# Kernel tuning notes

Measured on AMD Instinct MI355X. Metric: run time of the kernel, lower is better.

Reference implementation:

```python
import jax, jax.numpy as jnp
import numpy as np

B, L, D = 4, 8192, 512
H, G = 8, 4
DH = D // H      # head channels = 64
GC = D // G      # group channels = 128
KSZ = 5          # kernel = offset_range_factor
PAD = KSZ // 2   # = 2; applied to BOTH offset convs (second conv has k=1, pad=2 -> length L+4)


def conv1d(x, w, b, pad):
    # x: (N, Cin, L), w: (Cout, Cin, K) torch layout
    y = jax.lax.conv_general_dilated(x, w, (1,), [(pad, pad)],
                                     dimension_numbers=('NCH', 'OIH', 'NCH'))
    return y + b[None, :, None]


def setup_inputs() -> dict:
    key = jax.random.key(0)
    ks = jax.random.split(key, 9)
    s = 0.02
    p = lambda k, shape: jax.random.normal(k, shape, jnp.float32) * s
    return {
        'x': jax.random.normal(ks[0], (B, L, D), jnp.float32),
        'Wq': p(ks[1], (D, D)), 'bq': jnp.zeros((D,), jnp.float32),
        'Wk': p(ks[2], (D, D)), 'bk': jnp.zeros((D,), jnp.float32),
        'Wv': p(ks[3], (D, D)), 'bv': jnp.zeros((D,), jnp.float32),
        'Woff1': p(ks[4], (GC, GC, KSZ)), 'boff1': jnp.zeros((GC,), jnp.float32),
        'Woff2': p(ks[5], (1, GC, 1)), 'boff2': jnp.zeros((1,), jnp.float32),
        'rel_bias': p(ks[6], (1, D, L)),
        'Wout': p(ks[7], (D, D)), 'bout': jnp.zeros((D,), jnp.float32),
    }


def reference(x, Wq, bq, Wk, bk, Wv, bv, Woff1, boff1, Woff2, boff2, rel_bias, Wout, bout):
    Bv, Lv, Dv = x.shape
    xc = jnp.transpose(x, (0, 2, 1))                         # (B, D, L)
    # 1x1 convs == pointwise linear over channels
    q = jnp.einsum('od,bdl->bol', Wq, xc) + bq[None, :, None]
    # offset prediction on grouped queries
    gq = q.reshape(Bv * G, GC, Lv)                            # (BG, GC, L)
    o = conv1d(gq, Woff1, boff1, PAD)                         # (BG, GC, L)
    o = conv1d(o, Woff2, boff2, PAD)                          # (BG, 1, L+4) due to k=1,pad=2
    offset = jnp.tanh(o[:, 0, :]) * KSZ                       # (BG, L+4)
    n = offset.shape[-1]
    vgrid = jnp.arange(n, dtype=x.dtype) + offset             # (BG, L+4)
    g = 2.0 * vgrid / (n - 1) - 1.0                           # normalized to [-1, 1] over n
    # torch grid_sample, align_corners=False, padding_mode='zeros', H = L
    pos = ((g + 1.0) * Lv - 1.0) / 2.0
    p0 = jnp.floor(pos)
    w1 = pos - p0                                             # weight for upper neighbor
    p0i = p0.astype(jnp.int32)
    p1i = p0i + 1
    feats = xc.reshape(Bv * G, GC, Lv)

    def gather(idx):
        valid = ((idx >= 0) & (idx < Lv)).astype(x.dtype)      # (BG, n)
        idxc = jnp.clip(idx, 0, Lv - 1)
        vals = jnp.take_along_axis(feats, idxc[:, None, :].astype(jnp.int32).repeat(1, axis=1), axis=2) if False else jnp.take_along_axis(feats, jnp.broadcast_to(idxc[:, None, :], (Bv * G, GC, n)), axis=2)
        return vals * valid[:, None, :]

    samp = gather(p0i) * (1.0 - w1)[:, None, :] + gather(p1i) * w1[:, None, :]
    x_sampled = samp[:, :, :Lv].reshape(Bv, Dv, Lv)           # (B, D, L)
    k = jnp.einsum('od,bdl->bol', Wk, x_sampled) + bk[None, :, None]
    v = jnp.einsum('od,bdl->bol', Wv, x_sampled) + bv[None, :, None] + rel_bias
    qh = q.reshape(Bv * H, DH, Lv)
    kh = k.reshape(Bv * H, DH, Lv)
    vh = v.reshape(Bv * H, DH, Lv)
    # channel-attention: contraction over sequence length L
    scores = jnp.einsum('bil,bjl->bij', qh, kh) * (Dv ** -0.5)  # (B*H, DH, DH)
    attn = jax.nn.softmax(scores, axis=-1)
    out = jnp.einsum('bij,bjl->bil', attn, vh)                # (B*H, DH, L)
    # rearrange '(b g) l c -> b c (g l)' with b=B, g=H, l=DH, c=L -> (B, L, D)
    out = jnp.transpose(out.reshape(Bv, H, DH, Lv), (0, 3, 1, 2)).reshape(Bv, Lv, H * DH)
    return out @ Wout.T + bout
```

## Files before the change

### kernel.cpp

```cpp
#include <hip/hip_runtime.h>
#include <hip/hip_bf16.h>
#include <math.h>

using u16 = unsigned short;
using u32 = unsigned int;

typedef __attribute__((ext_vector_type(8))) short s16x8;
typedef __attribute__((ext_vector_type(4))) float f32x4;

#define B_  4
#define L_  8192
#define D_  512
#define H_  8
#define G_  4

__device__ __forceinline__ float bf2f(u16 u) {
    u32 x = ((u32)u) << 16;
    return __uint_as_float(x);
}
__device__ __forceinline__ u16 f2bf(float f) {
    u32 x = __float_as_uint(f);
    u32 lsb = (x >> 16) & 1u;
    x += 0x7FFFu + lsb;
    return (u16)(x >> 16);
}
__device__ __forceinline__ void async16(const void* g, void* l) {
    __builtin_amdgcn_global_load_lds((const __attribute__((address_space(1))) u32*)g,
                                     (__attribute__((address_space(3))) u32*)l, 16, 0, 0);
}

#define CAST_BLOCKS 16384
#define PACK_BLOCKS 384
__global__ __launch_bounds__(256) void prep_kernel(const float* __restrict__ x,
                                                   u16* __restrict__ x_bf,
                                                   const float* __restrict__ Wq,
                                                   const float* __restrict__ Wk,
                                                   const float* __restrict__ Wv,
                                                   u16* __restrict__ Pq,
                                                   u16* __restrict__ Pk,
                                                   u16* __restrict__ Pv,
                                                   const float* __restrict__ W1,
                                                   const float* __restrict__ b1,
                                                   const float* __restrict__ W2,
                                                   const float* __restrict__ b2,
                                                   float* __restrict__ weff) {
    const int bid = blockIdx.x;
    const int tid = threadIdx.x;
    if (bid < CAST_BLOCKS) {
        const int i = bid * 256 + tid;
        float4 v = ((const float4*)x)[i];
        ushort4 o;
        o.x = f2bf(v.x); o.y = f2bf(v.y); o.z = f2bf(v.z); o.w = f2bf(v.w);
        ((ushort4*)x_bf)[i] = o;
    } else if (bid < CAST_BLOCKS + PACK_BLOCKS) {
        const int pb = bid - CAST_BLOCKS;
        const int wsel = pb >> 7;
        const int xb = pb & 127;
        const int g = xb * 4 + (tid >> 6);
        const int lane = tid & 63;
        const int cb = g >> 4, kc = g & 15;
        const int q = lane >> 4, fm = lane & 15;
        const float* W = (wsel == 0) ? Wq : (wsel == 1) ? Wk : Wv;
        u16* P = (wsel == 0) ? Pq : (wsel == 1) ? Pk : Pv;
        const float* src = W + (size_t)(cb * 16 + fm) * 512 + kc * 32 + q * 8;
        float4 a = *(const float4*)src;
        float4 b = *(const float4*)(src + 4);
        ushort4 o0, o1;
        o0.x = f2bf(a.x); o0.y = f2bf(a.y); o0.z = f2bf(a.z); o0.w = f2bf(a.w);
        o1.x = f2bf(b.x); o1.y = f2bf(b.y); o1.z = f2bf(b.z); o1.w = f2bf(b.w);
        u16* dst = P + (size_t)g * 512 + lane * 8;
        *(ushort4*)dst = o0;
        *(ushort4*)(dst + 4) = o1;
    } else {
        const int idx = (bid - CAST_BLOCKS - PACK_BLOCKS) * 256 + tid;
        if (idx < 640) {
            int cin = idx / 5, dk = idx % 5;
            float acc = 0.f;
            for (int c = 0; c < 128; ++c) acc += W2[c] * W1[(c * 128 + cin) * 5 + dk];
            weff[idx] = acc;
        } else if (idx == 640) {
            float s = b2[0];
            for (int c = 0; c < 128; ++c) s += W2[c] * b1[c];
            weff[640] = s;
        } else if (idx == 641) {
            weff[641] = b2[0];
        }
    }
}

__global__ __launch_bounds__(256) void offsets_kernel(const u16* __restrict__ qT,
                                                      const float* __restrict__ weff,
                                                      int* __restrict__ p0o,
                                                      float* __restrict__ w1o) {
    __shared__ u16 qs[128 * 72];
    __shared__ float wf[642];
    __shared__ float red[4][64];
    const int tid = threadIdx.x;
    const int t0 = blockIdx.x * 64;
    const int bg = blockIdx.y;
    const int b = bg >> 2, g = bg & 3;
    for (int i = tid; i < 642; i += 256) wf[i] = weff[i];
    for (int i = tid; i < 128 * 9; i += 256) {
        const int ch = i / 9, seg = i - ch * 9;
        const int l = t0 - 8 + seg * 8;
        s16x8 val = {0, 0, 0, 0, 0, 0, 0, 0};
        if (l >= 0)
            val = *(const s16x8*)(qT + (size_t)(b * D_ + g * 128 + ch) * L_ + l);
        *(s16x8*)(qs + ch * 72 + seg * 8) = val;
    }
    __syncthreads();
    const int w = tid >> 6, lane = tid & 63;
    float acc = 0.f;
    for (int c = 0; c < 32; ++c) {
        const int ch = w * 32 + c;
        const u16* row = qs + ch * 72 + lane + 4;
        const float* wr = wf + ch * 5;
        #pragma unroll
        for (int dk = 0; dk < 5; ++dk) acc += wr[dk] * bf2f(row[dk]);
    }
    red[w][lane] = acc;
    __syncthreads();
    if (w == 0) {
        const float s = red[0][lane] + red[1][lane] + red[2][lane] + red[3][lane];
        const int t = t0 + lane;
        const float o2 = (t >= 2) ? (s + wf[640]) : wf[641];
        const double offv = tanh((double)o2) * 5.0;
        const double vg  = (double)t + offv;
        const double gg  = 2.0 * vg / 8195.0 - 1.0;
        const double pos = ((gg + 1.0) * 8192.0 - 1.0) * 0.5;
        const double p0d = floor(pos);
        p0o[(size_t)bg * L_ + t] = (int)p0d;
        w1o[(size_t)bg * L_ + t] = (float)(pos - p0d);
    }
}

__global__ __launch_bounds__(256) void sample_bf16(const u16* __restrict__ xb,
                                                   const int* __restrict__ p0i,
                                                   const float* __restrict__ w1f,
                                                   u16* __restrict__ xs) {
    const size_t idx = (size_t)blockIdx.x * 256 + threadIdx.x;
    const int d8 = (int)(idx & 63);
    const int t = (int)((idx >> 6) & 8191);
    const int b = (int)(idx >> 19);
    const int g = d8 >> 4;
    const size_t og = (size_t)(b * 4 + g) * L_ + t;
    const int p0 = p0i[og];
    const float w1 = w1f[og];
    const float w0 = 1.f - w1;
    const int p1 = p0 + 1;
    s16x8 a = {0, 0, 0, 0, 0, 0, 0, 0}, c = {0, 0, 0, 0, 0, 0, 0, 0};
    if (p0 >= 0 && p0 < L_) a = *(const s16x8*)(xb + ((size_t)b * L_ + p0) * D_ + d8 * 8);
    if (p1 >= 0 && p1 < L_) c = *(const s16x8*)(xb + ((size_t)b * L_ + p1) * D_ + d8 * 8);
    u16 o[8];
    #pragma unroll
    for (int j = 0; j < 8; ++j)
        o[j] = f2bf(bf2f(((const u16*)&a)[j]) * w0 + bf2f(((const u16*)&c)[j]) * w1);
    *(s16x8*)(xs + idx * 8) = *(const s16x8*)o;
}

__global__ __launch_bounds__(256) void sample_f32(const float* __restrict__ x,
                                                  const int* __restrict__ p0i,
                                                  const float* __restrict__ w1f,
                                                  u16* __restrict__ xs) {
    const size_t idx4 = (size_t)blockIdx.x * 256 + threadIdx.x;
    const int d4 = (int)(idx4 & 127);
    const int t = (int)((idx4 >> 7) & 8191);
    const int b = (int)(idx4 >> 20);
    const int g = d4 >> 5;
    const size_t og = (size_t)(b * 4 + g) * L_ + t;
    const int p0 = p0i[og];
    const float w1 = w1f[og];
    const float w0 = 1.f - w1;
    const int p1 = p0 + 1;
    float4 v0 = {0.f, 0.f, 0.f, 0.f}, v1 = {0.f, 0.f, 0.f, 0.f};
    if (p0 >= 0 && p0 < L_) v0 = *(const float4*)(x + ((size_t)b * L_ + p0) * D_ + d4 * 4);
    if (p1 >= 0 && p1 < L_) v1 = *(const float4*)(x + ((size_t)b * L_ + p1) * D_ + d4 * 4);
    ushort4 o;
    o.x = f2bf(v0.x * w0 + v1.x * w1);
    o.y = f2bf(v0.y * w0 + v1.y * w1);
    o.z = f2bf(v0.z * w0 + v1.z * w1);
    o.w = f2bf(v0.w * w0 + v1.w * w1);
    ((ushort4*)xs)[idx4] = o;
}

template <int MODE>
__global__ __launch_bounds__(256) void gemm_kernel(const u16* __restrict__ A,
                                                   const u16* __restrict__ P0,
                                                   const u16* __restrict__ P1,
                                                   const float* __restrict__ bias0,
                                                   const float* __restrict__ bias1,
                                                   const float* __restrict__ rel,
                                                   void* __restrict__ out0,
                                                   void* __restrict__ out1) {
    __shared__ __align__(16) short abuf[2][128 * 32];
    const int tid = threadIdx.x;
    const int wave = tid >> 6, lane = tid & 63;
    const int bid = blockIdx.x;
    const int xcd = bid & 7;
    const int kk_ = bid >> 3;
    int r0, c0, sel;
    if (MODE == 1) { r0 = (xcd * 32 + (kk_ >> 3)) * 128; sel = (kk_ >> 2) & 1; c0 = (kk_ & 3) * 128; }
    else           { r0 = (xcd * 32 + (kk_ >> 2)) * 128; sel = 0;              c0 = (kk_ & 3) * 128; }
    const u16* P = (MODE == 1 && sel) ? P1 : P0;
    if (MODE == 2) P += (size_t)(r0 >> 13) * 262144;
    const float* bias = (MODE == 1 && sel) ? bias1 : bias0;
    void* out = (MODE == 1 && sel) ? out1 : out0;

    const int wm = (wave >> 1) * 64, wn = (wave & 1) * 64;
    const int srow = lane >> 2;
    const int scol = ((lane & 3) ^ ((srow >> 1) & 3)) * 8;
    const u16* gA = A + (size_t)(r0 + wave * 32) * D_ + scol;
    const int cbase = (c0 + wn) >> 4;

    f32x4 acc[4][4];
    #pragma unroll
    for (int mi = 0; mi < 4; ++mi)
        #pragma unroll
        for (int ni = 0; ni < 4; ++ni) acc[mi][ni] = (f32x4){0.f, 0.f, 0.f, 0.f};

    const int fm = lane & 15;
    const int sblk = ((lane >> 4) ^ ((fm >> 1) & 3)) * 8;

    s16x8 bfrag[4];

    auto stageA = [&](int bsel, int it) {
        const int k0 = it * 32;
        #pragma unroll
        for (int j = 0; j < 2; ++j)
            async16(gA + (size_t)(j * 16 + srow) * D_ + k0,
                    &abuf[bsel][wave * 1024 + j * 512]);
    };
    auto loadB = [&](int it) {
        #pragma unroll
        for (int ni = 0; ni < 4; ++ni)
            bfrag[ni] = *(const s16x8*)(P + ((size_t)((cbase + ni) * 16 + it) * 64 + lane) * 8);
    };

    stageA(0, 0);
    __syncthreads();

    #pragma unroll
    for (int it = 0; it < 16; ++it) {
        const int cur = it & 1;
        loadB(it);
        if (it < 15) stageA(cur ^ 1, it + 1);
        s16x8 af[4];
        #pragma unroll
        for (int mi = 0; mi < 4; ++mi)
            af[mi] = *(const s16x8*)(&abuf[cur][(wm + mi * 16 + fm) * 32 + sblk]);
        #pragma unroll
        for (int mi = 0; mi < 4; ++mi)
            #pragma unroll
            for (int ni = 0; ni < 4; ++ni)
                acc[mi][ni] = __builtin_amdgcn_mfma_f32_16x16x32_bf16(af[mi], bfrag[ni], acc[mi][ni], 0, 0, 0);
        __syncthreads();
    }

    const int fn = lane & 15;
    const int q4 = (lane >> 4) * 4;
    const bool transposed = (MODE == 0) || (MODE == 1 && sel == 0);
    #pragma unroll
    for (int mi = 0; mi < 4; ++mi) {
        #pragma unroll
        for (int ni = 0; ni < 4; ++ni) {
            const int c = c0 + wn + ni * 16 + fn;
            const float bsum = bias[c];
            if (MODE == 2) {
                #pragma unroll
                for (int rg = 0; rg < 4; ++rg) {
                    const int r = r0 + wm + mi * 16 + q4 + rg;
                    ((float*)out)[(size_t)r * D_ + c] = acc[mi][ni][rg] + bsum;
                }
            } else if (transposed) {
                const int r_ = r0 + wm + mi * 16 + q4;
                const int bb = r_ >> 13;
                const int l  = r_ & (L_ - 1);
                ushort4 o;
                o.x = f2bf(acc[mi][ni][0] + bsum);
                o.y = f2bf(acc[mi][ni][1] + bsum);
                o.z = f2bf(acc[mi][ni][2] + bsum);
                o.w = f2bf(acc[mi][ni][3] + bsum);
                *(ushort4*)((u16*)out + (size_t)(bb * D_ + c) * L_ + l) = o;
            } else {
                const int r_ = r0 + wm + mi * 16 + q4;
                const int l  = r_ & (L_ - 1);
                const float4 rl = *(const float4*)(rel + (size_t)c * L_ + l);
                ((u16*)out)[(size_t)(r_ + 0) * D_ + c] = f2bf(acc[mi][ni][0] + bsum + rl.x);
                ((u16*)out)[(size_t)(r_ + 1) * D_ + c] = f2bf(acc[mi][ni][1] + bsum + rl.y);
                ((u16*)out)[(size_t)(r_ + 2) * D_ + c] = f2bf(acc[mi][ni][2] + bsum + rl.z);
                ((u16*)out)[(size_t)(r_ + 3) * D_ + c] = f2bf(acc[mi][ni][3] + bsum + rl.w);
            }
        }
    }
}

__global__ __launch_bounds__(256) void scores_partial(const u16* __restrict__ qT,
                                                      const u16* __restrict__ kT,
                                                      float* __restrict__ part) {
    __shared__ u16 qs[64 * 136];
    __shared__ u16 ks[64 * 136];
    const int chunk = blockIdx.x;
    const int bh = blockIdx.y;
    const int b = bh >> 3, h = bh & 7;
    const int tid = threadIdx.x;
    const int wave = tid >> 6, lane = tid & 63;
    const int wr = (wave >> 1) * 32;
    const int wc = (wave & 1) * 32;
    f32x4 acc[2][2];
    #pragma unroll
    for (int mi = 0; mi < 2; ++mi)
        #pragma unroll
        for (int ni = 0; ni < 2; ++ni) acc[mi][ni] = (f32x4){0.f, 0.f, 0.f, 0.f};
    const size_t base = (size_t)(b * D_ + h * 64) * L_;
    const int m = lane & 15, q = lane >> 4;
    for (int iter = 0; iter < 4; ++iter) {
        const int l0 = chunk * 512 + iter * 128;
        __syncthreads();
        for (int i = tid; i < 1024; i += 256) {
            const int lb = i & 15, ch = i >> 4;
            const size_t gidx = base + (size_t)ch * L_ + l0 + lb * 8;
            *(s16x8*)(qs + ch * 136 + lb * 8) = *(const s16x8*)(qT + gidx);
            *(s16x8*)(ks + ch * 136 + lb * 8) = *(const s16x8*)(kT + gidx);
        }
        __syncthreads();
        #pragma unroll
        for (int kst = 0; kst < 4; ++kst) {
            const int kk = kst * 32 + q * 8;
            s16x8 af[2], bfr[2];
            af[0]  = *(const s16x8*)(qs + (wr + m) * 136 + kk);
            af[1]  = *(const s16x8*)(qs + (wr + 16 + m) * 136 + kk);
            bfr[0] = *(const s16x8*)(ks + (wc + m) * 136 + kk);
            bfr[1] = *(const s16x8*)(ks + (wc + 16 + m) * 136 + kk);
            #pragma unroll
            for (int mi = 0; mi < 2; ++mi)
                #pragma unroll
                for (int ni = 0; ni < 2; ++ni)
                    acc[mi][ni] = __builtin_amdgcn_mfma_f32_16x16x32_bf16(af[mi], bfr[ni], acc[mi][ni], 0, 0, 0);
        }
    }
    float* dst = part + (size_t)(bh * 16 + chunk) * 4096;
    const int q4 = (lane >> 4) * 4;
    #pragma unroll
    for (int mi = 0; mi < 2; ++mi) {
        #pragma unroll
        for (int ni = 0; ni < 2; ++ni) {
            const int j = wc + ni * 16 + m;
            #pragma unroll
            for (int rg = 0; rg < 4; ++rg) {
                const int i = wr + mi * 16 + q4 + rg;
                dst[i * 64 + j] = acc[mi][ni][rg];
            }
        }
    }
}

__global__ __launch_bounds__(256) void softmax_kernel(const float* __restrict__ part,
                                                      float* __restrict__ attn) {
    const int tid = threadIdx.x;
    const int wave = tid >> 6, lane = tid & 63;
    const int row = blockIdx.x * 4 + wave;
    const int bh = row >> 6, i = row & 63;
    float s = 0.f;
    #pragma unroll
    for (int c = 0; c < 16; ++c) s += part[((size_t)(bh * 16 + c)) * 4096 + i * 64 + lane];
    s *= 0.04419417382415922f;
    float m = s;
    for (int off = 32; off > 0; off >>= 1) m = fmaxf(m, __shfl_xor(m, off));
    float e = expf(s - m);
    float sum = e;
    for (int off = 32; off > 0; off >>= 1) sum += __shfl_xor(sum, off);
    attn[(size_t)bh * 4096 + i * 64 + lane] = e / sum;
}

__global__ __launch_bounds__(256) void build_M(const float* __restrict__ Wout,
                                               const float* __restrict__ attn,
                                               u16* __restrict__ Mpack) {
    const int idx = blockIdx.x * 256 + threadIdx.x;
    const int col = idx & 511;
    const int o = (idx >> 9) & 511;
    const int b = idx >> 18;
    const int h = col >> 6, j0 = col & 63;
    const float* wr = Wout + o * 512 + h * 64;
    const float* ar = attn + (size_t)(b * H_ + h) * 4096 + j0;
    float s = 0.f;
    #pragma unroll 8
    for (int i = 0; i < 64; ++i) s += wr[i] * ar[i * 64];
    const int cb = o >> 4, fm = o & 15;
    const int kc = col >> 5, q = (col >> 3) & 3, j = col & 7;
    Mpack[(size_t)b * 262144 + ((size_t)(cb * 16 + kc) * 64 + q * 16 + fm) * 8 + j] = f2bf(s);
}

extern "C" void kernel_launch(void* const* d_in, const int* in_sizes, int n_in,
                              void* d_out, int out_size, void* d_ws, size_t ws_size,
                              hipStream_t stream) {
    const float* x    = (const float*)d_in[0];
    const float* Wq   = (const float*)d_in[1];
    const float* bq   = (const float*)d_in[2];
    const float* Wk   = (const float*)d_in[3];
    const float* bk   = (const float*)d_in[4];
    const float* Wv   = (const float*)d_in[5];
    const float* bv   = (const float*)d_in[6];
    const float* Wo1  = (const float*)d_in[7];
    const float* bo1  = (const float*)d_in[8];
    const float* Wo2  = (const float*)d_in[9];
    const float* bo2  = (const float*)d_in[10];
    const float* rel  = (const float*)d_in[11];
    const float* Wout = (const float*)d_in[12];
    const float* bout = (const float*)d_in[13];

    char* ws = (char*)d_ws;
    const size_t MB = 1024ull * 1024ull;
    const bool big = ws_size >= 165ull * MB;

    u16* x_bf = (u16*)(ws);
    u16* qT   = (u16*)(ws + 32 * MB);
    u16* kT   = (u16*)(ws + 64 * MB);
    u16* v_bf = (u16*)(ws + 96 * MB);

    u16*   xs;
    u16*   Pq; u16* Pk; u16* Pv;
    float* weff; int* p0i; float* w1f;
    float* part; float* attn; u16* Mpack;

    if (big) {
        xs    = (u16*)(ws + 128 * MB);
        part  = (float*)(ws + 128 * MB);
        attn  = (float*)((char*)part + 8 * MB);
        Mpack = (u16*)((char*)attn + 524288);
        Pq    = (u16*)(ws + 160 * MB);
        Pk    = Pq + 262144;
        Pv    = Pk + 262144;
        weff  = (float*)(ws + 162 * MB);
        p0i   = (int*)(ws + 162 * MB + 65536);
        w1f   = (float*)((char*)p0i + 524288);
    } else {
        xs    = x_bf;
        Pq    = (u16*)(ws + 128 * MB);
        Pk    = Pq + 262144;
        Pv    = Pk + 262144;
        weff  = (float*)(ws + 130 * MB);
        p0i   = (int*)(ws + 130 * MB + 65536);
        w1f   = (float*)((char*)p0i + 524288);
        part  = (float*)((char*)w1f + 524288);
        attn  = (float*)((char*)part + 8 * MB);
        Mpack = (u16*)((char*)attn + 524288);
    }

    prep_kernel<<<CAST_BLOCKS + PACK_BLOCKS + 3, 256, 0, stream>>>(
        x, x_bf, Wq, Wk, Wv, Pq, Pk, Pv, Wo1, bo1, Wo2, bo2, weff);
    gemm_kernel<0><<<1024, 256, 0, stream>>>(x_bf, Pq, nullptr, bq, nullptr, nullptr, (void*)qT, nullptr);
    offsets_kernel<<<dim3(128, 16), 256, 0, stream>>>(qT, weff, p0i, w1f);
    if (big) sample_bf16<<<8192, 256, 0, stream>>>(x_bf, p0i, w1f, xs);
    else     sample_f32<<<16384, 256, 0, stream>>>(x, p0i, w1f, xs);
    gemm_kernel<1><<<2048, 256, 0, stream>>>(xs, Pk, Pv, bk, bv, rel, (void*)kT, (void*)v_bf);
    scores_partial<<<dim3(16, 32), 256, 0, stream>>>(qT, kT, part);
    softmax_kernel<<<512, 256, 0, stream>>>(part, attn);
    build_M<<<4096, 256, 0, stream>>>(Wout, attn, Mpack);
    gemm_kernel<2><<<1024, 256, 0, stream>>>(v_bf, Mpack, nullptr, bout, nullptr, nullptr, d_out, nullptr);
}
```

Measured before the change: 382.1 us.

## Stage B tiles through LDS with a 4-slot async pipeline in projection GEMM

The GEMM kernel now copies the packed weight (B) fragments into LDS with async global-to-LDS loads instead of reading them directly into registers each iteration. It also deepens the A/B staging from double buffering to a 4-slot ring that keeps three stages in flight, using explicit vmcnt waits plus raw barriers in place of __syncthreads. The goal is to hide global load latency and share B fragments across waves. In exchange LDS use roughly quadruples, which may lower occupancy, and the hand-coded waitcnt values must exactly match the number of outstanding loads.

```diff
diff --git a/kernel.cpp b/kernel.cpp
--- a/kernel.cpp
+++ b/kernel.cpp
@@ -28,6 +28,9 @@
     __builtin_amdgcn_global_load_lds((const __attribute__((address_space(1))) u32*)g,
                                      (__attribute__((address_space(3))) u32*)l, 16, 0, 0);
 }
+#define WAIT_VM8   0x0F78
+#define WAIT_VM4   0x0F74
+#define WAIT_VM0   0x0F70
 
 #define CAST_BLOCKS 16384
 #define PACK_BLOCKS 384
@@ -192,7 +195,8 @@
                                                    const float* __restrict__ rel,
                                                    void* __restrict__ out0,
                                                    void* __restrict__ out1) {
-    __shared__ __align__(16) short abuf[2][128 * 32];
+    __shared__ __align__(16) short abuf[4][128 * 32];
+    __shared__ __align__(16) short bbuf[4][128 * 32];
     const int tid = threadIdx.x;
     const int wave = tid >> 6, lane = tid & 63;
     const int bid = blockIdx.x;
@@ -210,7 +214,7 @@
     const int srow = lane >> 2;
     const int scol = ((lane & 3) ^ ((srow >> 1) & 3)) * 8;
     const u16* gA = A + (size_t)(r0 + wave * 32) * D_ + scol;
-    const int cbase = (c0 + wn) >> 4;
+    const int cb0 = c0 >> 4;
 
     f32x4 acc[4][4];
     #pragma unroll
@@ -221,39 +225,44 @@
     const int fm = lane & 15;
     const int sblk = ((lane >> 4) ^ ((fm >> 1) & 3)) * 8;
 
-    s16x8 bfrag[4];
-
-    auto stageA = [&](int bsel, int it) {
+    auto stageAB = [&](int slot, int it) {
         const int k0 = it * 32;
         #pragma unroll
         for (int j = 0; j < 2; ++j)
             async16(gA + (size_t)(j * 16 + srow) * D_ + k0,
-                    &abuf[bsel][wave * 1024 + j * 512]);
+                    &abuf[slot][wave * 1024 + j * 512]);
+        #pragma unroll
+        for (int j = 0; j < 2; ++j)
+            async16(P + ((size_t)((cb0 + wave * 2 + j) * 16 + it) * 64 + lane) * 8,
+                    &bbuf[slot][(wave * 2 + j) * 512]);
     };
-    auto loadB = [&](int it) {
+
+    stageAB(0, 0); stageAB(1, 1); stageAB(2, 2);
+    __builtin_amdgcn_s_waitcnt(WAIT_VM8);
+    __builtin_amdgcn_s_barrier();
+
+    #pragma unroll
+    for (int it = 0; it < 16; ++it) {
+        const int slot = it & 3;
+        s16x8 af[4], bf[4];
+        #pragma unroll
+        for (int mi = 0; mi < 4; ++mi)
+            af[mi] = *(const s16x8*)(&abuf[slot][(wm + mi * 16 + fm) * 32 + sblk]);
         #pragma unroll
         for (int ni = 0; ni < 4; ++ni)
-            bfrag[ni] = *(const s16x8*)(P + ((size_t)((cbase + ni) * 16 + it) * 64 + lane) * 8);
-    };
-
-    stageA(0, 0);
-    __syncthreads();
-
-    #pragma unroll
-    for (int it = 0; it < 16; ++it) {
-        const int cur = it & 1;
-        loadB(it);
-        if (it < 15) stageA(cur ^ 1, it + 1);
-        s16x8 af[4];
-        #pragma unroll
-        for (int mi = 0; mi < 4; ++mi)
-            af[mi] = *(const s16x8*)(&abuf[cur][(wm + mi * 16 + fm) * 32 + sblk]);
+            bf[ni] = *(const s16x8*)(&bbuf[slot][((wave & 1) * 4 + ni) * 512 + lane * 8]);
+        if (it < 13) stageAB((it + 3) & 3, it + 3);
         #pragma unroll
         for (int mi = 0; mi < 4; ++mi)
             #pragma unroll
             for (int ni = 0; ni < 4; ++ni)
-                acc[mi][ni] = __builtin_amdgcn_mfma_f32_16x16x32_bf16(af[mi], bfrag[ni], acc[mi][ni], 0, 0, 0);
-        __syncthreads();
+                acc[mi][ni] = __builtin_amdgcn_mfma_f32_16x16x32_bf16(af[mi], bf[ni], acc[mi][ni], 0, 0, 0);
+        if (it < 15) {
+            if (it <= 12)      __builtin_amdgcn_s_waitcnt(WAIT_VM8);
+            else if (it == 13) __builtin_amdgcn_s_waitcnt(WAIT_VM4);
+            else               __builtin_amdgcn_s_waitcnt(WAIT_VM0);
+            __builtin_amdgcn_s_barrier();
+        }
     }
 
     const int fn = lane & 15;
```

After: 375.9 us. Within noise of the previous version (-1.6%).

## Widen GEMM tiles, fuse K and V outputs per block, double K-step

Applied to the files above, without the earlier changes.

The GEMM kernel now computes K and V projections in the same block from one staged A tile, so the sampled input is read once instead of twice. Modes 0 and 2 use 128x256 tiles with 8 N-fragments per wave, and every mode stages 64 K-columns per iteration in two sub-buffers, which halves the number of barriers. Grids shrink to match. The cost is many more accumulator registers per wave (128 f32x4 lanes' worth), which lowers occupancy and may cause spills. Shared memory per block also doubles.

```diff
diff --git a/kernel.cpp b/kernel.cpp
--- a/kernel.cpp
+++ b/kernel.cpp
@@ -192,86 +192,107 @@
                                                    const float* __restrict__ rel,
                                                    void* __restrict__ out0,
                                                    void* __restrict__ out1) {
-    __shared__ __align__(16) short abuf[2][128 * 32];
+    __shared__ __align__(16) short abuf[2][2][128 * 32];
     const int tid = threadIdx.x;
     const int wave = tid >> 6, lane = tid & 63;
     const int bid = blockIdx.x;
     const int xcd = bid & 7;
     const int kk_ = bid >> 3;
-    int r0, c0, sel;
-    if (MODE == 1) { r0 = (xcd * 32 + (kk_ >> 3)) * 128; sel = (kk_ >> 2) & 1; c0 = (kk_ & 3) * 128; }
-    else           { r0 = (xcd * 32 + (kk_ >> 2)) * 128; sel = 0;              c0 = (kk_ & 3) * 128; }
-    const u16* P = (MODE == 1 && sel) ? P1 : P0;
-    if (MODE == 2) P += (size_t)(r0 >> 13) * 262144;
-    const float* bias = (MODE == 1 && sel) ? bias1 : bias0;
-    void* out = (MODE == 1 && sel) ? out1 : out0;
-
-    const int wm = (wave >> 1) * 64, wn = (wave & 1) * 64;
+    int r0, c0;
+    if (MODE == 1) { r0 = (xcd * 32 + (kk_ >> 2)) * 128; c0 = (kk_ & 3) * 128; }
+    else           { r0 = (xcd * 32 + (kk_ >> 1)) * 128; c0 = (kk_ & 1) * 256; }
+    const u16* Pk = P0;
+    if (MODE == 2) Pk += (size_t)(r0 >> 13) * 262144;
+    const u16* Pv = P1;
+
+    const int wm = (wave >> 1) * 64;
+    const int wn = (MODE == 1) ? (wave & 1) * 64 : (wave & 1) * 128;
+    constexpr int NI = (MODE == 1) ? 4 : 8;
+    const int cbase = (c0 + wn) >> 4;
+
     const int srow = lane >> 2;
     const int scol = ((lane & 3) ^ ((srow >> 1) & 3)) * 8;
     const u16* gA = A + (size_t)(r0 + wave * 32) * D_ + scol;
-    const int cbase = (c0 + wn) >> 4;
-
-    f32x4 acc[4][4];
-    #pragma unroll
-    for (int mi = 0; mi < 4; ++mi)
-        #pragma unroll
-        for (int ni = 0; ni < 4; ++ni) acc[mi][ni] = (f32x4){0.f, 0.f, 0.f, 0.f};
-
     const int fm = lane & 15;
     const int sblk = ((lane >> 4) ^ ((fm >> 1) & 3)) * 8;
 
-    s16x8 bfrag[4];
-
-    auto stageA = [&](int bsel, int it) {
-        const int k0 = it * 32;
-        #pragma unroll
-        for (int j = 0; j < 2; ++j)
-            async16(gA + (size_t)(j * 16 + srow) * D_ + k0,
-                    &abuf[bsel][wave * 1024 + j * 512]);
-    };
-    auto loadB = [&](int it) {
-        #pragma unroll
-        for (int ni = 0; ni < 4; ++ni)
-            bfrag[ni] = *(const s16x8*)(P + ((size_t)((cbase + ni) * 16 + it) * 64 + lane) * 8);
+    f32x4 acc[4][NI];
+    #pragma unroll
+    for (int mi = 0; mi < 4; ++mi)
+        #pragma unroll
+        for (int ni = 0; ni < NI; ++ni) acc[mi][ni] = (f32x4){0.f, 0.f, 0.f, 0.f};
+    f32x4 accv[4][(MODE == 1) ? 4 : 1];
+    if (MODE == 1) {
+        #pragma unroll
+        for (int mi = 0; mi < 4; ++mi)
+            #pragma unroll
+            for (int ni = 0; ni < 4; ++ni) accv[mi][ni] = (f32x4){0.f, 0.f, 0.f, 0.f};
+    }
+
+    auto stageA = [&](int buf, int it) {
+        #pragma unroll
+        for (int sub = 0; sub < 2; ++sub)
+            #pragma unroll
+            for (int j = 0; j < 2; ++j)
+                async16(gA + (size_t)(j * 16 + srow) * D_ + it * 64 + sub * 32,
+                        &abuf[buf][sub][wave * 1024 + j * 512]);
     };
 
     stageA(0, 0);
     __syncthreads();
 
     #pragma unroll
-    for (int it = 0; it < 16; ++it) {
+    for (int it = 0; it < 8; ++it) {
         const int cur = it & 1;
-        loadB(it);
-        if (it < 15) stageA(cur ^ 1, it + 1);
-        s16x8 af[4];
-        #pragma unroll
-        for (int mi = 0; mi < 4; ++mi)
-            af[mi] = *(const s16x8*)(&abuf[cur][(wm + mi * 16 + fm) * 32 + sblk]);
-        #pragma unroll
-        for (int mi = 0; mi < 4; ++mi)
-            #pragma unroll
-            for (int ni = 0; ni < 4; ++ni)
-                acc[mi][ni] = __builtin_amdgcn_mfma_f32_16x16x32_bf16(af[mi], bfrag[ni], acc[mi][ni], 0, 0, 0);
+        if (it < 7) stageA(cur ^ 1, it + 1);
+        #pragma unroll
+        for (int sub = 0; sub < 2; ++sub) {
+            const int kc = it * 2 + sub;
+            s16x8 bk[NI];
+            #pragma unroll
+            for (int ni = 0; ni < NI; ++ni)
+                bk[ni] = *(const s16x8*)(Pk + ((size_t)((cbase + ni) * 16 + kc) * 64 + lane) * 8);
+            s16x8 bv[(MODE == 1) ? 4 : 1];
+            if (MODE == 1) {
+                #pragma unroll
+                for (int ni = 0; ni < 4; ++ni)
+                    bv[ni] = *(const s16x8*)(Pv + ((size_t)((cbase + ni) * 16 + kc) * 64 + lane) * 8);
+            }
+            s16x8 af[4];
+            #pragma unroll
+            for (int mi = 0; mi < 4; ++mi)
+                af[mi] = *(const s16x8*)(&abuf[cur][sub][(wm + mi * 16 + fm) * 32 + sblk]);
+            #pragma unroll
+            for (int mi = 0; mi < 4; ++mi)
+                #pragma unroll
+                for (int ni = 0; ni < NI; ++ni)
+                    acc[mi][ni] = __builtin_amdgcn_mfma_f32_16x16x32_bf16(af[mi], bk[ni], acc[mi][ni], 0, 0, 0);
+            if (MODE == 1) {
+                #pragma unroll
+                for (int mi = 0; mi < 4; ++mi)
+                    #pragma unroll
+                    for (int ni = 0; ni < 4; ++ni)
+                        accv[mi][ni] = __builtin_amdgcn_mfma_f32_16x16x32_bf16(af[mi], bv[ni], accv[mi][ni], 0, 0, 0);
+            }
+        }
         __syncthreads();
     }
 
     const int fn = lane & 15;
     const int q4 = (lane >> 4) * 4;
-    const bool transposed = (MODE == 0) || (MODE == 1 && sel == 0);
     #pragma unroll
     for (int mi = 0; mi < 4; ++mi) {
         #pragma unroll
-        for (int ni = 0; ni < 4; ++ni) {
+        for (int ni = 0; ni < NI; ++ni) {
             const int c = c0 + wn + ni * 16 + fn;
-            const float bsum = bias[c];
+            const float bsum = bias0[c];
             if (MODE == 2) {
                 #pragma unroll
                 for (int rg = 0; rg < 4; ++rg) {
                     const int r = r0 + wm + mi * 16 + q4 + rg;
-                    ((float*)out)[(size_t)r * D_ + c] = acc[mi][ni][rg] + bsum;
+                    ((float*)out0)[(size_t)r * D_ + c] = acc[mi][ni][rg] + bsum;
                 }
-            } else if (transposed) {
+            } else {
                 const int r_ = r0 + wm + mi * 16 + q4;
                 const int bb = r_ >> 13;
                 const int l  = r_ & (L_ - 1);
@@ -280,15 +301,24 @@
                 o.y = f2bf(acc[mi][ni][1] + bsum);
                 o.z = f2bf(acc[mi][ni][2] + bsum);
                 o.w = f2bf(acc[mi][ni][3] + bsum);
-                *(ushort4*)((u16*)out + (size_t)(bb * D_ + c) * L_ + l) = o;
-            } else {
+                *(ushort4*)((u16*)out0 + (size_t)(bb * D_ + c) * L_ + l) = o;
+            }
+        }
+    }
+    if (MODE == 1) {
+        #pragma unroll
+        for (int mi = 0; mi < 4; ++mi) {
+            #pragma unroll
+            for (int ni = 0; ni < 4; ++ni) {
+                const int c = c0 + wn + ni * 16 + fn;
+                const float bsum = bias1[c];
                 const int r_ = r0 + wm + mi * 16 + q4;
                 const int l  = r_ & (L_ - 1);
                 const float4 rl = *(const float4*)(rel + (size_t)c * L_ + l);
-                ((u16*)out)[(size_t)(r_ + 0) * D_ + c] = f2bf(acc[mi][ni][0] + bsum + rl.x);
-                ((u16*)out)[(size_t)(r_ + 1) * D_ + c] = f2bf(acc[mi][ni][1] + bsum + rl.y);
-                ((u16*)out)[(size_t)(r_ + 2) * D_ + c] = f2bf(acc[mi][ni][2] + bsum + rl.z);
-                ((u16*)out)[(size_t)(r_ + 3) * D_ + c] = f2bf(acc[mi][ni][3] + bsum + rl.w);
+                ((u16*)out1)[(size_t)(r_ + 0) * D_ + c] = f2bf(accv[mi][ni][0] + bsum + rl.x);
+                ((u16*)out1)[(size_t)(r_ + 1) * D_ + c] = f2bf(accv[mi][ni][1] + bsum + rl.y);
+                ((u16*)out1)[(size_t)(r_ + 2) * D_ + c] = f2bf(accv[mi][ni][2] + bsum + rl.z);
+                ((u16*)out1)[(size_t)(r_ + 3) * D_ + c] = f2bf(accv[mi][ni][3] + bsum + rl.w);
             }
         }
     }
@@ -448,13 +478,13 @@
 
     prep_kernel<<<CAST_BLOCKS + PACK_BLOCKS + 3, 256, 0, stream>>>(
         x, x_bf, Wq, Wk, Wv, Pq, Pk, Pv, Wo1, bo1, Wo2, bo2, weff);
-    gemm_kernel<0><<<1024, 256, 0, stream>>>(x_bf, Pq, nullptr, bq, nullptr, nullptr, (void*)qT, nullptr);
+    gemm_kernel<0><<<512, 256, 0, stream>>>(x_bf, Pq, nullptr, bq, nullptr, nullptr, (void*)qT, nullptr);
     offsets_kernel<<<dim3(128, 16), 256, 0, stream>>>(qT, weff, p0i, w1f);
     if (big) sample_bf16<<<8192, 256, 0, stream>>>(x_bf, p0i, w1f, xs);
     else     sample_f32<<<16384, 256, 0, stream>>>(x, p0i, w1f, xs);
-    gemm_kernel<1><<<2048, 256, 0, stream>>>(xs, Pk, Pv, bk, bv, rel, (void*)kT, (void*)v_bf);
+    gemm_kernel<1><<<1024, 256, 0, stream>>>(xs, Pk, Pv, bk, bv, rel, (void*)kT, (void*)v_bf);
     scores_partial<<<dim3(16, 32), 256, 0, stream>>>(qT, kT, part);
     softmax_kernel<<<512, 256, 0, stream>>>(part, attn);
     build_M<<<4096, 256, 0, stream>>>(Wout, attn, Mpack);
-    gemm_kernel<2><<<1024, 256, 0, stream>>>(v_bf, Mpack, nullptr, bout, nullptr, nullptr, d_out, nullptr);
-}
+    gemm_kernel<2><<<512, 256, 0, stream>>>(v_bf, Mpack, nullptr, bout, nullptr, nullptr, d_out, nullptr);
+}
```

Result: slower. 409.5 us (+7.2%).
